# Optimization experiments

Measured on AMD Instinct MI355X. Metric: run time of the kernel, lower is better.

Reference implementation:

```python
import jax, jax.numpy as jnp
import numpy as np

V, E, H, H2, T, B, S = 50000, 300, 512, 256, 10, 64, 256
START_IDX, STOP_IDX = 8, 9


def setup_inputs() -> dict:
    key = jax.random.key(0)
    ks = jax.random.split(key, 16)
    sd = 1.0 / np.sqrt(H2)
    inp = {
        'sentence': jax.random.randint(ks[0], (B, S), 0, V, dtype=jnp.int32),
        'emb': jax.random.normal(ks[1], (V, E), jnp.float32),
        'wih_f': jax.random.uniform(ks[2], (4 * H2, E), jnp.float32, -sd, sd),
        'whh_f': jax.random.uniform(ks[3], (4 * H2, H2), jnp.float32, -sd, sd),
        'bih_f': jax.random.uniform(ks[4], (4 * H2,), jnp.float32, -sd, sd),
        'bhh_f': jax.random.uniform(ks[5], (4 * H2,), jnp.float32, -sd, sd),
        'wih_b': jax.random.uniform(ks[6], (4 * H2, E), jnp.float32, -sd, sd),
        'whh_b': jax.random.uniform(ks[7], (4 * H2, H2), jnp.float32, -sd, sd),
        'bih_b': jax.random.uniform(ks[8], (4 * H2,), jnp.float32, -sd, sd),
        'bhh_b': jax.random.uniform(ks[9], (4 * H2,), jnp.float32, -sd, sd),
        'W_out': jax.random.uniform(ks[10], (T, H), jnp.float32, -1.0 / np.sqrt(H), 1.0 / np.sqrt(H)),
        'b_out': jax.random.uniform(ks[11], (T,), jnp.float32, -1.0 / np.sqrt(H), 1.0 / np.sqrt(H)),
        'h0': jax.random.normal(ks[12], (2, B, H2), jnp.float32),
        'c0': jax.random.normal(ks[13], (2, B, H2), jnp.float32),
    }
    trans = jax.random.normal(ks[14], (T, T), jnp.float32)
    trans = trans.at[START_IDX, :].set(-10000.0).at[:, STOP_IDX].set(-10000.0)
    inp['transitions'] = trans
    return inp


def _lstm_dir(x, h0, c0, wih, whh, bih, bhh, reverse):
    # x: (S, B, E); returns hidden states (S, B, H2)
    def step(carry, xt):
        h, c = carry
        g = xt @ wih.T + bih + h @ whh.T + bhh  # (B, 4*H2)
        i, f, gg, o = jnp.split(g, 4, axis=-1)  # PyTorch gate order i,f,g,o
        c = jax.nn.sigmoid(f) * c + jax.nn.sigmoid(i) * jnp.tanh(gg)
        h = jax.nn.sigmoid(o) * jnp.tanh(c)
        return (h, c), h
    _, hs = jax.lax.scan(step, (h0, c0), x, reverse=reverse)
    return hs


def _features(sentence, emb, wih_f, whh_f, bih_f, bhh_f, wih_b, whh_b, bih_b, bhh_b,
              W_out, b_out, h0, c0):
    # Replicate torch's .view(seq,batch,-1): raw memory reinterpretation of (B,S,E)
    embeds = emb[sentence].reshape(S, B, E)
    h_f = _lstm_dir(embeds, h0[0], c0[0], wih_f, whh_f, bih_f, bhh_f, False)
    h_b = _lstm_dir(embeds, h0[1], c0[1], wih_b, whh_b, bih_b, bhh_b, True)
    lstm_out = jnp.concatenate([h_f, h_b], axis=-1)  # (S, B, H)
    # Replicate torch's .view(batch,-1,hidden): reinterpretation, not transpose
    lstm_out = lstm_out.reshape(B, S, H)
    return lstm_out @ W_out.T + b_out  # (B, S, T)


def _viterbi(feats, transitions):
    # feats: (B, S, T)
    init = jnp.full((B, T), -10000.0, feats.dtype).at[:, START_IDX].set(0.0)

    def step(fv, feat_t):
        # ntv[b, next, prev] = fv[b, prev] + transitions[next, prev]
        ntv = fv[:, None, :] + transitions[None, :, :]
        vv = jnp.max(ntv, axis=2)          # (B, T)
        bp = jnp.argmax(ntv, axis=2)       # (B, T) backpointers
        return vv + feat_t, bp

    fv, bps = jax.lax.scan(step, init, jnp.swapaxes(feats, 0, 1))  # bps: (S, B, T)
    terminal = fv + transitions[STOP_IDX]
    path_score = jnp.max(terminal, axis=1)[:, None]   # (B, 1)
    last_tag = jnp.argmax(terminal, axis=1)           # (B,)

    def back(best, bp):
        return bp[jnp.arange(B), best], best

    _, path = jax.lax.scan(back, last_tag, bps, reverse=True)  # (S, B)
    return path_score, path.T  # (B, 1), (B, S)


def reference(sentence, emb, wih_f, whh_f, bih_f, bhh_f, wih_b, whh_b, bih_b, bhh_b,
              W_out, b_out, transitions, h0, c0):
    feats = _features(sentence, emb, wih_f, whh_f, bih_f, bhh_f,
                      wih_b, whh_b, bih_b, bhh_b, W_out, b_out, h0, c0)
    return _viterbi(feats, transitions)
```

## Files before the change

### kernel.cpp

```cpp
#include <hip/hip_runtime.h>

#define E_    300
#define H2_   256
#define B_    64
#define S_    256
#define G_    (S_*B_)
#define GATES (4*H2_)
#define KREG  64
#define WP4   49
#define HP    260

__global__ void prep_kernel(const float* __restrict__ whh_f, const float* __restrict__ whh_b,
                            const float* __restrict__ bih_f, const float* __restrict__ bhh_f,
                            const float* __restrict__ bih_b, const float* __restrict__ bhh_b,
                            float* __restrict__ wpack, float* __restrict__ bsum) {
    int idx = blockIdx.x * blockDim.x + threadIdx.x;
    if (idx < 2 * 8 * 128 * 256) {
        int d  = idx >> 18;
        int s  = (idx >> 15) & 7;
        int rr = (idx >> 8) & 127;
        int k  = idx & 255;
        int r  = ((rr >> 5) << 8) + s * 32 + (rr & 31);
        const float* w = d ? whh_b : whh_f;
        wpack[idx] = w[r * H2_ + k];
    }
    if (idx < 2 * GATES) {
        int d = idx >> 10, j = idx & 1023;
        bsum[idx] = d ? (bih_b[j] + bhh_b[j]) : (bih_f[j] + bhh_f[j]);
    }
}

__global__ __launch_bounds__(256) void xproj_kernel(
    const int* __restrict__ sent, const float* __restrict__ emb,
    const float* __restrict__ wih_f, const float* __restrict__ wih_b,
    const float* __restrict__ bsum, float* __restrict__ xp) {
    __shared__ float As[128 * 21];
    __shared__ float Bs[20 * 64];
    __shared__ int   toks[128];
    int gt = blockIdx.x, jt = blockIdx.y, d = blockIdx.z;
    const float* wih = d ? wih_b : wih_f;
    int tid = threadIdx.x;
    int g0 = gt * 128, j0 = jt * 64;
    if (tid < 128) toks[tid] = sent[g0 + tid];
    __syncthreads();

    int ty = tid >> 4, tx = tid & 15;
    float acc[8][4];
    float4 bv = *(const float4*)&bsum[d * 1024 + j0 + tx * 4];
    #pragma unroll
    for (int i = 0; i < 8; i++) { acc[i][0] = bv.x; acc[i][1] = bv.y; acc[i][2] = bv.z; acc[i][3] = bv.w; }

    for (int kt = 0; kt < 15; kt++) {
        int k0 = kt * 20;
        #pragma unroll
        for (int l = 0; l < 10; l++) {
            int e = l * 256 + tid; int i = e / 20, k = e % 20;
            As[i * 21 + k] = emb[(long)toks[i] * E_ + k0 + k];
        }
        #pragma unroll
        for (int l = 0; l < 5; l++) {
            int e = l * 256 + tid; int k = e >> 6, j = e & 63;
            Bs[k * 64 + j] = wih[(j0 + j) * E_ + k0 + k];
        }
        __syncthreads();
        #pragma unroll
        for (int k = 0; k < 20; k++) {
            float4 b4 = *(const float4*)&Bs[k * 64 + tx * 4];
            #pragma unroll
            for (int i = 0; i < 8; i++) {
                float a = As[(ty * 8 + i) * 21 + k];
                acc[i][0] += a * b4.x; acc[i][1] += a * b4.y;
                acc[i][2] += a * b4.z; acc[i][3] += a * b4.w;
            }
        }
        __syncthreads();
    }
    #pragma unroll
    for (int i = 0; i < 8; i++) {
        float4 o; o.x = acc[i][0]; o.y = acc[i][1]; o.z = acc[i][2]; o.w = acc[i][3];
        *(float4*)&xp[((long)d * G_ + g0 + ty * 8 + i) * 1024 + j0 + tx * 4] = o;
    }
}

__global__ __launch_bounds__(512, 2) void lstm_kernel(
    const float* __restrict__ xp, const float* __restrict__ wpack,
    const float* __restrict__ h0, const float* __restrict__ c0,
    float* __restrict__ hcat, unsigned long long* __restrict__ mbox) {
    __shared__ float4 wlds[128 * WP4];
    __shared__ float  h_lds[4 * HP];
    __shared__ float  g_stage[512];

    int t = threadIdx.x;
    int bid = blockIdx.x;
    int x = bid & 7, rest = bid >> 3;
    int s = rest & 7, Ghi = rest >> 3;
    int G = Ghi * 8 + x;
    int d = G >> 4, bg = G & 15;
    int j = t & 3, rr = t >> 2;
    int q = rr >> 5, uu = rr & 31;
    int r = q * 256 + s * 32 + uu;
    int b = bg * 4 + j;

    const float* wp = wpack + (size_t)((d * 8 + s) * 128) * 256;

    float4 wr[16];
    #pragma unroll
    for (int kk = 0; kk < 16; kk++) wr[kk] = ((const float4*)(wp + rr * 256))[kk];

    for (int e = t; e < 128 * 48; e += 512) {
        int rrow = e / 48, kk = e % 48;
        wlds[rrow * WP4 + kk] = ((const float4*)(wp + rrow * 256 + KREG))[kk];
    }
    for (int e = t; e < 1024; e += 512) {
        int jj = e >> 8, u = e & 255;
        h_lds[jj * HP + u] = h0[(d * B_ + bg * 4 + jj) * H2_ + u];
    }
    float c = 0.f;
    if (t < 128) c = c0[(d * B_ + b) * H2_ + s * 32 + uu];

    unsigned long long* mb_out = mbox + (size_t)(G * 8 + s) * 256;
    const float* xq = xp + (size_t)d * G_ * 1024 + r;
    float xcur;
    {
        int s0 = d ? 255 : 0;
        xcur = xq[(size_t)(s0 * 64 + b) * 1024];
    }
    __syncthreads();

    for (int step = 0; step < S_; step++) {
        float xnext = 0.f;
        int sn = d ? (254 - step) : (step + 1);
        if (step < 255) xnext = xq[(size_t)(sn * 64 + b) * 1024];

        const float4* hj = (const float4*)&h_lds[j * HP];
        float a0 = xcur, a1 = 0.f, a2 = 0.f, a3 = 0.f;
        #pragma unroll
        for (int kk = 0; kk < 16; kk++) {
            float4 hv = hj[kk];
            a0 += wr[kk].x * hv.x; a1 += wr[kk].y * hv.y;
            a2 += wr[kk].z * hv.z; a3 += wr[kk].w * hv.w;
        }
        const float4* wrow = &wlds[rr * WP4];
        #pragma unroll
        for (int kk = 0; kk < 48; kk++) {
            float4 wv = wrow[kk]; float4 hv = hj[16 + kk];
            a0 += wv.x * hv.x; a1 += wv.y * hv.y;
            a2 += wv.z * hv.z; a3 += wv.w * hv.w;
        }
        g_stage[t] = (a0 + a1) + (a2 + a3);
        __syncthreads();

        int sidx = d ? (255 - step) : step;
        if (t < 128) {
            float iv = g_stage[t],        fv = g_stage[128 + t];
            float gv = g_stage[256 + t],  ov = g_stage[384 + t];
            float si = 1.f / (1.f + __expf(-iv));
            float sf = 1.f / (1.f + __expf(-fv));
            float so = 1.f / (1.f + __expf(-ov));
            float tg = tanhf(gv);
            c = sf * c + si * tg;
            float h = so * tanhf(c);
            h_lds[j * HP + s * 32 + uu] = h;
            union { float f; unsigned u; } cv; cv.f = h;
            __hip_atomic_store(&mb_out[(step & 1) * 128 + t],
                               ((unsigned long long)(unsigned)(step + 1) << 32) | cv.u,
                               __ATOMIC_RELAXED, __HIP_MEMORY_SCOPE_AGENT);
            hcat[(size_t)(sidx * 64 + b) * 512 + d * 256 + s * 32 + uu] = h;
        } else {
            int v = t - 128;
            #pragma unroll
            for (int it = 0; it < 3; it++) {
                int vv = v + it * 384;
                if (vv < 896) {
                    int spr = vv >> 7;
                    int sp = spr + (spr >= s ? 1 : 0);
                    int w = vv & 127;
                    unsigned long long* ad =
                        mbox + (size_t)(G * 8 + sp) * 256 + (step & 1) * 128 + w;
                    unsigned long long val;
                    do {
                        val = __hip_atomic_load(ad, __ATOMIC_RELAXED, __HIP_MEMORY_SCOPE_AGENT);
                    } while ((unsigned)(val >> 32) != (unsigned)(step + 1));
                    union { unsigned u; float f; } cv; cv.u = (unsigned)val;
                    h_lds[(w & 3) * HP + sp * 32 + (w >> 2)] = cv.f;
                }
            }
        }
        __syncthreads();
        xcur = xnext;
    }
}

__global__ void feats_kernel(const float* __restrict__ hcat, const float* __restrict__ Wout,
                             const float* __restrict__ bout, float* __restrict__ feats) {
    int tid = threadIdx.x; int w = tid >> 6, l = tid & 63;
    int g = blockIdx.x * 4 + w;
    float r[8];
    #pragma unroll
    for (int m = 0; m < 8; m++) r[m] = hcat[(long)g * 512 + m * 64 + l];
    #pragma unroll
    for (int tt = 0; tt < 10; tt++) {
        float a = 0.f;
        #pragma unroll
        for (int m = 0; m < 8; m++) a += r[m] * Wout[tt * 512 + m * 64 + l];
        #pragma unroll
        for (int off = 32; off > 0; off >>= 1) a += __shfl_down(a, off);
        if (l == 0) feats[g * 10 + tt] = a + bout[tt];
    }
}

__global__ void viterbi_kernel(const float* __restrict__ feats, const float* __restrict__ trans,
                               float* __restrict__ out) {
    __shared__ unsigned char bp[256 * 16];
    int l = threadIdx.x; int b = blockIdx.x;
    float trrow[10];
    #pragma unroll
    for (int p = 0; p < 10; p++) trrow[p] = (l < 10) ? trans[l * 10 + p] : 0.f;
    float tr_stop = (l < 10) ? trans[90 + l] : -3e38f;
    float fv = (l == 8) ? 0.f : -10000.f;

    for (int s = 0; s < 256; s++) {
        float m = -3e38f; int arg = 0;
        #pragma unroll
        for (int p = 0; p < 10; p++) {
            float v = __shfl(fv, p) + trrow[p];
            if (v > m) { m = v; arg = p; }
        }
        float ft = (l < 10) ? feats[((long)b * 256 + s) * 10 + l] : 0.f;
        fv = m + ft;
        if (l < 10) bp[s * 16 + l] = (unsigned char)arg;
    }
    __syncthreads();
    float term = fv + tr_stop;
    float best = -3e38f; int bt = 0;
    #pragma unroll
    for (int p = 0; p < 10; p++) {
        float v = __shfl(term, p);
        if (v > best) { best = v; bt = p; }
    }
    if (l == 0) {
        out[b] = best;
        int cur = bt;
        out[64 + b * 256 + 255] = (float)cur;
        for (int s = 254; s >= 0; s--) {
            cur = bp[(s + 1) * 16 + cur];
            out[64 + b * 256 + s] = (float)cur;
        }
    }
}

extern "C" void kernel_launch(void* const* d_in, const int* in_sizes, int n_in,
                              void* d_out, int out_size, void* d_ws, size_t ws_size,
                              hipStream_t stream) {
    const int*   sent  = (const int*)  d_in[0];
    const float* emb   = (const float*)d_in[1];
    const float* wih_f = (const float*)d_in[2];
    const float* whh_f = (const float*)d_in[3];
    const float* bih_f = (const float*)d_in[4];
    const float* bhh_f = (const float*)d_in[5];
    const float* wih_b = (const float*)d_in[6];
    const float* whh_b = (const float*)d_in[7];
    const float* bih_b = (const float*)d_in[8];
    const float* bhh_b = (const float*)d_in[9];
    const float* Wout  = (const float*)d_in[10];
    const float* bout  = (const float*)d_in[11];
    const float* h0    = (const float*)d_in[12];
    const float* c0    = (const float*)d_in[13];
    const float* trans = (const float*)d_in[14];

    float* ws    = (float*)d_ws;
    float* xp    = ws;
    float* hcat  = ws + 33554432;
    float* wpack = ws + 41943040;
    float* bsum  = ws + 42467328;
    unsigned long long* mbox = (unsigned long long*)(ws + 42469376);
    float* feats = ws;
    float* out   = (float*)d_out;

    hipLaunchKernelGGL(prep_kernel, dim3(2048), dim3(256), 0, stream,
                       whh_f, whh_b, bih_f, bhh_f, bih_b, bhh_b, wpack, bsum);
    hipLaunchKernelGGL(xproj_kernel, dim3(128, 16, 2), dim3(256), 0, stream,
                       sent, emb, wih_f, wih_b, bsum, xp);

    void* lstm_args[] = { (void*)&xp, (void*)&wpack, (void*)&h0, (void*)&c0,
                          (void*)&hcat, (void*)&mbox };
    hipLaunchCooperativeKernel((const void*)lstm_kernel, dim3(256), dim3(512),
                               lstm_args, 0, stream);

    hipLaunchKernelGGL(feats_kernel, dim3(4096), dim3(256), 0, stream,
                       hcat, Wout, bout, feats);
    hipLaunchKernelGGL(viterbi_kernel, dim3(64), dim3(64), 0, stream,
                       feats, trans, out);
}
```

Measured before the change: 1.537 ms.

## Keep all recurrent weights in registers with K-split partial sums in LSTM kernel

Repacks the recurrent weight matrix so each thread holds a 4-gate by 16-column weight slice entirely in registers, which removes the LDS weight reads. Each thread computes partial dot products for all 4 batch rows and writes them to a shared partial buffer. 128 threads then reduce the 16 K-chunks, gather the gates with shuffles, and update c/h. This adds a reduction pass through shared memory and drops the prefetch of the next step's x projection, so the global load latency now sits on the critical path.

```diff
diff --git a/kernel.cpp b/kernel.cpp
--- a/kernel.cpp
+++ b/kernel.cpp
@@ -6,23 +6,24 @@
 #define S_    256
 #define G_    (S_*B_)
 #define GATES (4*H2_)
-#define KREG  64
-#define WP4   49
-#define HP    260
+#define NS    8
 
 __global__ void prep_kernel(const float* __restrict__ whh_f, const float* __restrict__ whh_b,
                             const float* __restrict__ bih_f, const float* __restrict__ bhh_f,
                             const float* __restrict__ bih_b, const float* __restrict__ bhh_b,
                             float* __restrict__ wpack, float* __restrict__ bsum) {
     int idx = blockIdx.x * blockDim.x + threadIdx.x;
-    if (idx < 2 * 8 * 128 * 256) {
+    if (idx < 2 * 8 * 512 * 64) {
         int d  = idx >> 18;
         int s  = (idx >> 15) & 7;
-        int rr = (idx >> 8) & 127;
-        int k  = idx & 255;
-        int r  = ((rr >> 5) << 8) + s * 32 + (rr & 31);
+        int t  = (idx >> 6) & 511;
+        int e  = idx & 63;
+        int gt = e >> 4, kk = e & 15;
+        int u  = t >> 4, cc = t & 15;
+        int row = gt * 256 + s * 32 + u;
+        int col = cc * 16 + kk;
         const float* w = d ? whh_b : whh_f;
-        wpack[idx] = w[r * H2_ + k];
+        wpack[idx] = w[row * H2_ + col];
     }
     if (idx < 2 * GATES) {
         int d = idx >> 10, j = idx & 1023;
@@ -86,9 +87,8 @@
     const float* __restrict__ xp, const float* __restrict__ wpack,
     const float* __restrict__ h0, const float* __restrict__ c0,
     float* __restrict__ hcat, unsigned long long* __restrict__ mbox) {
-    __shared__ float4 wlds[128 * WP4];
-    __shared__ float  h_lds[4 * HP];
-    __shared__ float  g_stage[512];
+    __shared__ float h_cur[4 * 320];
+    __shared__ float part[4 * 2180];
 
     int t = threadIdx.x;
     int bid = blockIdx.x;
@@ -96,98 +96,124 @@
     int s = rest & 7, Ghi = rest >> 3;
     int G = Ghi * 8 + x;
     int d = G >> 4, bg = G & 15;
-    int j = t & 3, rr = t >> 2;
-    int q = rr >> 5, uu = rr & 31;
-    int r = q * 256 + s * 32 + uu;
-    int b = bg * 4 + j;
-
-    const float* wp = wpack + (size_t)((d * 8 + s) * 128) * 256;
-
-    float4 wr[16];
-    #pragma unroll
-    for (int kk = 0; kk < 16; kk++) wr[kk] = ((const float4*)(wp + rr * 256))[kk];
-
-    for (int e = t; e < 128 * 48; e += 512) {
-        int rrow = e / 48, kk = e % 48;
-        wlds[rrow * WP4 + kk] = ((const float4*)(wp + rrow * 256 + KREG))[kk];
-    }
+
+    float4 w[4][4];
+    const float4* wbase = (const float4*)(wpack + (size_t)((d * 8 + s) * 512 + t) * 64);
+    #pragma unroll
+    for (int gt = 0; gt < 4; gt++)
+        #pragma unroll
+        for (int k4 = 0; k4 < 4; k4++)
+            w[gt][k4] = wbase[gt * 4 + k4];
+
+    int fu = t >> 4, fcc = t & 15;
+    int rgt = t & 3, ru = t >> 2;
+
     for (int e = t; e < 1024; e += 512) {
-        int jj = e >> 8, u = e & 255;
-        h_lds[jj * HP + u] = h0[(d * B_ + bg * 4 + jj) * H2_ + u];
-    }
-    float c = 0.f;
-    if (t < 128) c = c0[(d * B_ + b) * H2_ + s * 32 + uu];
-
-    unsigned long long* mb_out = mbox + (size_t)(G * 8 + s) * 256;
-    const float* xq = xp + (size_t)d * G_ * 1024 + r;
-    float xcur;
-    {
-        int s0 = d ? 255 : 0;
-        xcur = xq[(size_t)(s0 * 64 + b) * 1024];
-    }
+        int j = e >> 8, k = e & 255;
+        h_cur[j * 320 + (k >> 4) * 20 + (k & 15)] = h0[(d * B_ + bg * 4 + j) * H2_ + k];
+    }
+    float c[4] = {0.f, 0.f, 0.f, 0.f};
+    if (t < 128 && rgt == 0) {
+        #pragma unroll
+        for (int j = 0; j < 4; j++)
+            c[j] = c0[(d * B_ + bg * 4 + j) * H2_ + s * 32 + ru];
+    }
+    unsigned long long* mb_out = mbox + (size_t)(G * NS + s) * 256;
+    const size_t xbase = (size_t)d * G_ * 1024;
     __syncthreads();
 
     for (int step = 0; step < S_; step++) {
-        float xnext = 0.f;
-        int sn = d ? (254 - step) : (step + 1);
-        if (step < 255) xnext = xq[(size_t)(sn * 64 + b) * 1024];
-
-        const float4* hj = (const float4*)&h_lds[j * HP];
-        float a0 = xcur, a1 = 0.f, a2 = 0.f, a3 = 0.f;
-        #pragma unroll
-        for (int kk = 0; kk < 16; kk++) {
-            float4 hv = hj[kk];
-            a0 += wr[kk].x * hv.x; a1 += wr[kk].y * hv.y;
-            a2 += wr[kk].z * hv.z; a3 += wr[kk].w * hv.w;
-        }
-        const float4* wrow = &wlds[rr * WP4];
-        #pragma unroll
-        for (int kk = 0; kk < 48; kk++) {
-            float4 wv = wrow[kk]; float4 hv = hj[16 + kk];
-            a0 += wv.x * hv.x; a1 += wv.y * hv.y;
-            a2 += wv.z * hv.z; a3 += wv.w * hv.w;
-        }
-        g_stage[t] = (a0 + a1) + (a2 + a3);
+        int sidx = d ? (255 - step) : step;
+        float xv[4] = {0.f, 0.f, 0.f, 0.f};
+        if (t < 128) {
+            #pragma unroll
+            for (int j = 0; j < 4; j++)
+                xv[j] = xp[xbase + (size_t)(sidx * 64 + bg * 4 + j) * 1024
+                           + rgt * 256 + s * 32 + ru];
+        }
+        float acc[4][4];
+        #pragma unroll
+        for (int gt = 0; gt < 4; gt++)
+            #pragma unroll
+            for (int j = 0; j < 4; j++) acc[gt][j] = 0.f;
+        #pragma unroll
+        for (int j = 0; j < 4; j++) {
+            const float* hb = &h_cur[j * 320 + fcc * 20];
+            #pragma unroll
+            for (int k4 = 0; k4 < 4; k4++) {
+                float4 h4 = *(const float4*)(hb + k4 * 4);
+                #pragma unroll
+                for (int gt = 0; gt < 4; gt++) {
+                    acc[gt][j] += w[gt][k4].x * h4.x + w[gt][k4].y * h4.y
+                                + w[gt][k4].z * h4.z + w[gt][k4].w * h4.w;
+                }
+            }
+        }
+        #pragma unroll
+        for (int gt = 0; gt < 4; gt++) {
+            float4 p; p.x = acc[gt][0]; p.y = acc[gt][1]; p.z = acc[gt][2]; p.w = acc[gt][3];
+            *(float4*)&part[gt * 2180 + fu * 68 + fcc * 4] = p;
+        }
         __syncthreads();
 
-        int sidx = d ? (255 - step) : step;
         if (t < 128) {
-            float iv = g_stage[t],        fv = g_stage[128 + t];
-            float gv = g_stage[256 + t],  ov = g_stage[384 + t];
-            float si = 1.f / (1.f + __expf(-iv));
-            float sf = 1.f / (1.f + __expf(-fv));
-            float so = 1.f / (1.f + __expf(-ov));
-            float tg = tanhf(gv);
-            c = sf * c + si * tg;
-            float h = so * tanhf(c);
-            h_lds[j * HP + s * 32 + uu] = h;
-            union { float f; unsigned u; } cv; cv.f = h;
-            __hip_atomic_store(&mb_out[(step & 1) * 128 + t],
-                               ((unsigned long long)(unsigned)(step + 1) << 32) | cv.u,
-                               __ATOMIC_RELAXED, __HIP_MEMORY_SCOPE_AGENT);
-            hcat[(size_t)(sidx * 64 + b) * 512 + d * 256 + s * 32 + uu] = h;
+            float4 sum; sum.x = xv[0]; sum.y = xv[1]; sum.z = xv[2]; sum.w = xv[3];
+            #pragma unroll
+            for (int cc = 0; cc < 16; cc++) {
+                float4 p = *(const float4*)&part[rgt * 2180 + ru * 68 + cc * 4];
+                sum.x += p.x; sum.y += p.y; sum.z += p.z; sum.w += p.w;
+            }
+            int lb = t & ~3;
+            float gi[4], gf[4], gg[4], go[4];
+            #pragma unroll
+            for (int j = 0; j < 4; j++) {
+                float v = (&sum.x)[j];
+                gi[j] = __shfl(v, lb + 0);
+                gf[j] = __shfl(v, lb + 1);
+                gg[j] = __shfl(v, lb + 2);
+                go[j] = __shfl(v, lb + 3);
+            }
+            if (rgt == 0) {
+                int u = ru, k = s * 32 + u;
+                #pragma unroll
+                for (int j = 0; j < 4; j++) {
+                    float si = 1.f / (1.f + __expf(-gi[j]));
+                    float sf = 1.f / (1.f + __expf(-gf[j]));
+                    float so = 1.f / (1.f + __expf(-go[j]));
+                    float tg = tanhf(gg[j]);
+                    c[j] = sf * c[j] + si * tg;
+                    float h = so * tanhf(c[j]);
+                    h_cur[j * 320 + (k >> 4) * 20 + (k & 15)] = h;
+                    union { float f; unsigned u32; } cv; cv.f = h;
+                    __hip_atomic_store(&mb_out[(step & 1) * 128 + j * 32 + u],
+                        ((unsigned long long)(unsigned)(step + 1) << 32) | cv.u32,
+                        __ATOMIC_RELAXED, __HIP_MEMORY_SCOPE_AGENT);
+                    hcat[(size_t)(sidx * 64 + bg * 4 + j) * 512 + d * 256 + k] = h;
+                }
+            }
         } else {
-            int v = t - 128;
-            #pragma unroll
-            for (int it = 0; it < 3; it++) {
-                int vv = v + it * 384;
+            int pt = t - 128;
+            #pragma unroll
+            for (int r = 0; r < 3; r++) {
+                int vv = pt + r * 384;
                 if (vv < 896) {
                     int spr = vv >> 7;
                     int sp = spr + (spr >= s ? 1 : 0);
-                    int w = vv & 127;
+                    int rem = vv & 127;
+                    int j = rem >> 5, u = rem & 31;
                     unsigned long long* ad =
-                        mbox + (size_t)(G * 8 + sp) * 256 + (step & 1) * 128 + w;
+                        mbox + (size_t)(G * NS + sp) * 256 + (step & 1) * 128 + rem;
                     unsigned long long val;
                     do {
                         val = __hip_atomic_load(ad, __ATOMIC_RELAXED, __HIP_MEMORY_SCOPE_AGENT);
                     } while ((unsigned)(val >> 32) != (unsigned)(step + 1));
-                    union { unsigned u; float f; } cv; cv.u = (unsigned)val;
-                    h_lds[(w & 3) * HP + sp * 32 + (w >> 2)] = cv.f;
+                    union { unsigned u32; float f; } cv; cv.u32 = (unsigned)val;
+                    int k = sp * 32 + u;
+                    h_cur[j * 320 + (k >> 4) * 20 + (k & 15)] = cv.f;
                 }
             }
         }
         __syncthreads();
-        xcur = xnext;
     }
 }
 
```

New measurement: 1.454 ms. 1.06x faster.
